# Performance work log

Measured on AMD Instinct MI355X. Metric: run time of the kernel, lower is better.

## Reference

```python
import jax, jax.numpy as jnp
import numpy as np

EPS = 1e-5
H = 128          # hidden_size
IN = 75          # input_size
T = 128          # seq len == window_size
B = 1024
OUT = 256        # lstm_output_size


def _bn(x, gamma, beta):
    # training-mode batch norm over the batch dim (biased variance, as in PyTorch BN)
    m = x.mean(axis=0)
    v = x.var(axis=0)
    return gamma * (x - m) * jax.lax.rsqrt(v + EPS) + beta


def _run_bnlstm_layer(xs, Wih, Whh, b, gih, bih, ghh, bhh, gc, bc):
    # xs: (T, B, D). Returns hidden stream (T, B, H).
    Bsz = xs.shape[1]
    h0 = jnp.zeros((Bsz, H), xs.dtype)
    c0 = jnp.zeros((Bsz, H), xs.dtype)

    def step(carry, x):
        h, c = carry
        gates = _bn(x @ Wih, gih, bih) + _bn(h @ Whh, ghh, bhh) + b  # (B, 4H)
        f, i, o, g = jnp.split(gates, 4, axis=1)                     # gate order f,i,o,g
        c1 = jax.nn.sigmoid(f) * c + jax.nn.sigmoid(i) * jnp.tanh(g)
        h1 = jax.nn.sigmoid(o) * jnp.tanh(_bn(c1, gc, bc))
        return (h1, c1), h1

    (_, _), hs = jax.lax.scan(step, (h0, c0), xs)
    return hs


def setup_inputs() -> dict:
    key = jax.random.key(0)
    ks = jax.random.split(key, 12)
    s = 0.05
    d = {
        'sequences': jax.random.normal(ks[0], (B, T, IN), jnp.float32),
        # layer 0 BNLSTM cell params (weights stored as (in, 4H) so y = x @ W)
        'Wih0': jax.random.normal(ks[1], (IN, 4 * H), jnp.float32) * s,
        'Whh0': jax.random.normal(ks[2], (H, 4 * H), jnp.float32) * s,
        'b0': jnp.zeros((4 * H,), jnp.float32),
        'gih0': jnp.full((4 * H,), 0.1, jnp.float32),
        'bih0': jnp.zeros((4 * H,), jnp.float32),
        'ghh0': jnp.full((4 * H,), 0.1, jnp.float32),
        'bhh0': jnp.zeros((4 * H,), jnp.float32),
        'gc0': jnp.full((H,), 0.1, jnp.float32),
        'bc0': jnp.zeros((H,), jnp.float32),
        # layer 1
        'Wih1': jax.random.normal(ks[3], (H, 4 * H), jnp.float32) * s,
        'Whh1': jax.random.normal(ks[4], (H, 4 * H), jnp.float32) * s,
        'b1': jnp.zeros((4 * H,), jnp.float32),
        'gih1': jnp.full((4 * H,), 0.1, jnp.float32),
        'bih1': jnp.zeros((4 * H,), jnp.float32),
        'ghh1': jnp.full((4 * H,), 0.1, jnp.float32),
        'bhh1': jnp.zeros((4 * H,), jnp.float32),
        'gc1': jnp.full((H,), 0.1, jnp.float32),
        'bc1': jnp.zeros((H,), jnp.float32),
        # fc: hidden -> lstm_output_size; decoder: lstm_output_size -> T*IN
        'fc_w': jax.random.normal(ks[5], (H, OUT), jnp.float32) * s,
        'fc_b': jnp.zeros((OUT,), jnp.float32),
        'dec_w': jax.random.normal(ks[6], (OUT, T * IN), jnp.float32) * s,
        'dec_b': jnp.zeros((T * IN,), jnp.float32),
    }
    return d


def reference(sequences, Wih0, Whh0, b0, gih0, bih0, ghh0, bhh0, gc0, bc0,
              Wih1, Whh1, b1, gih1, bih1, ghh1, bhh1, gc1, bc1,
              fc_w, fc_b, dec_w, dec_b):
    xs = jnp.transpose(sequences, (1, 0, 2))  # (T, B, IN), time-major
    hs0 = _run_bnlstm_layer(xs, Wih0, Whh0, b0, gih0, bih0, ghh0, bhh0, gc0, bc0)
    hs1 = _run_bnlstm_layer(hs0, Wih1, Whh1, b1, gih1, bih1, ghh1, bhh1, gc1, bc1)
    last = hs1[-1]                       # (B, H): last time step of top layer
    emb = last @ fc_w + fc_b             # (B, OUT)
    out = emb @ dec_w + dec_b            # (B, T*IN)
    return out.reshape(-1, T, IN)
```

## Files before the change

### kernel.cpp

```cpp
#include <hip/hip_runtime.h>
#include <stdint.h>
#include <stddef.h>

#define TT   128
#define BB   1024
#define INN  75
#define HH   128
#define KXP  96
#define OUTN 256
#define DECN 9600
#define EPSB 1e-5f

typedef short v8s __attribute__((ext_vector_type(8)));
typedef float v4f __attribute__((ext_vector_type(4)));
typedef unsigned short ush;
typedef unsigned int   u32;
typedef unsigned long long u64;

__device__ __align__(256) ush g_xpad[(size_t)TT * BB * KXP];
__device__ __align__(256) u64 g_h0s[(size_t)TT * BB * 32];
__device__ __align__(256) u64 g_h1s[(size_t)TT * BB * 32];
__device__ __align__(256) float g_c0[HH * BB];
__device__ __align__(256) float g_c1[HH * BB];
__device__ __align__(256) float g_P[(size_t)4 * 128 * 1024 * 4];
__device__ __align__(256) float g_pst[32 * 16 * 4 * 16 * 2];
__device__ __align__(256) ush g_wtih0[512 * KXP];
__device__ __align__(256) ush g_wthh0[512 * HH];
__device__ __align__(256) ush g_wtih1[512 * HH];
__device__ __align__(256) ush g_wthh1[512 * HH];
__device__ __align__(256) ush g_fcwt[OUTN * HH];
__device__ __align__(256) ush g_decwt[(size_t)DECN * OUTN];
__device__ __align__(256) ush g_emb[BB * OUTN];

__device__ __forceinline__ ush f2bf(float f) {
  u32 u = __float_as_uint(f);
  u32 r = (u + 0x7FFFu + ((u >> 16) & 1u)) >> 16;
  return (ush)r;
}
__device__ __forceinline__ float sigf(float x)  { return 1.f / (1.f + __expf(-x)); }
__device__ __forceinline__ float tanhf_(float x){ float e = __expf(2.f * x); return 1.f - 2.f / (e + 1.f); }
__device__ __forceinline__ v8s ld8(const ush* p) { return *reinterpret_cast<const v8s*>(p); }
__device__ __forceinline__ int origcol(int m) { return (m & 3) * 128 + (m >> 4) * 4 + ((m >> 2) & 3); }

__global__ void kpackx(const float* __restrict__ seq) {
  int idx = blockIdx.x * 256 + threadIdx.x;
  int kk = idx % KXP; int rest = idx / KXP;
  int b = rest % BB;  int t = rest / BB;
  float v = (kk < INN) ? seq[((size_t)b * TT + t) * INN + kk] : 0.f;
  g_xpad[idx] = f2bf(v);
}

__global__ void kpackw(const float* __restrict__ Wih0, const float* __restrict__ Whh0,
                       const float* __restrict__ Wih1, const float* __restrict__ Whh1,
                       const float* __restrict__ fcw,  const float* __restrict__ decw) {
  int idx = blockIdx.x * 256 + threadIdx.x;
  if (idx < 49152) {
    int m = idx / KXP, k = idx % KXP;
    g_wtih0[idx] = f2bf((k < INN) ? Wih0[k * 512 + origcol(m)] : 0.f);
  } else if (idx < 114688) {
    int j = idx - 49152; int m = j / HH, k = j % HH;
    g_wthh0[j] = f2bf(Whh0[k * 512 + origcol(m)]);
  } else if (idx < 180224) {
    int j = idx - 114688; int m = j / HH, k = j % HH;
    g_wtih1[j] = f2bf(Wih1[k * 512 + origcol(m)]);
  } else if (idx < 245760) {
    int j = idx - 180224; int m = j / HH, k = j % HH;
    g_wthh1[j] = f2bf(Whh1[k * 512 + origcol(m)]);
  } else if (idx < 278528) {
    int j = idx - 245760; int c = j / HH, k = j % HH;
    g_fcwt[j] = f2bf(fcw[k * OUTN + c]);
  } else {
    int j = idx - 278528; int n = j % DECN, k = j / DECN;
    g_decwt[(size_t)n * OUTN + k] = f2bf(decw[(size_t)k * DECN + n]);
  }
}

__global__ __launch_bounds__(256, 2) void kA(int s) {
  const int tid = threadIdx.x;
  const int wv = tid >> 6, l = tid & 63;
  const int lm = l & 15, lq = l >> 4;
  const int c = blockIdx.x & 31, r16 = blockIdx.x >> 5;
  const int R0 = r16 * 64 + wv * 16;
  const int row = R0 + lm;

  __shared__ float sred[4][16][8];

  const bool aL0 = (s < TT), ah0 = (s >= 1), ah1 = (s >= 2);
  const ush* const h0r = reinterpret_cast<const ush*>(g_h0s);
  const ush* const h1r = reinterpret_cast<const ush*>(g_h1s);

  v8s afx[3], af0[4], af1[4], af2[4];
#pragma unroll
  for (int ks = 0; ks < 3; ++ks)
    afx[ks] = ld8(&g_wtih0[(c * 16 + lm) * KXP + ks * 32 + lq * 8]);
#pragma unroll
  for (int ks = 0; ks < 4; ++ks) {
    af0[ks] = ld8(&g_wthh0[(c * 16 + lm) * HH + ks * 32 + lq * 8]);
    af1[ks] = ld8(&g_wtih1[(c * 16 + lm) * HH + ks * 32 + lq * 8]);
    af2[ks] = ld8(&g_wthh1[(c * 16 + lm) * HH + ks * 32 + lq * 8]);
  }

  const v4f vz = {0.f, 0.f, 0.f, 0.f};
  v4f Pi0 = vz, P0 = vz, P1 = vz, P2 = vz;

  if (aL0) {
    const ush* xp = g_xpad + ((size_t)s * BB + row) * KXP + lq * 8;
#pragma unroll
    for (int ks = 0; ks < 3; ++ks)
      Pi0 = __builtin_amdgcn_mfma_f32_16x16x32_bf16(afx[ks], ld8(xp + ks * 32), Pi0, 0, 0, 0);
  }
  if (ah0) {
    const ush* hp = h0r + ((size_t)(s - 1) * BB + row) * HH + lq * 8;
#pragma unroll
    for (int ks = 0; ks < 4; ++ks) {
      v8s b = ld8(hp + ks * 32);
      P0 = __builtin_amdgcn_mfma_f32_16x16x32_bf16(af0[ks], b, P0, 0, 0, 0);
      P1 = __builtin_amdgcn_mfma_f32_16x16x32_bf16(af1[ks], b, P1, 0, 0, 0);
    }
  }
  if (ah1) {
    const ush* hp = h1r + ((size_t)(s - 2) * BB + row) * HH + lq * 8;
#pragma unroll
    for (int ks = 0; ks < 4; ++ks)
      P2 = __builtin_amdgcn_mfma_f32_16x16x32_bf16(af2[ks], ld8(hp + ks * 32), P2, 0, 0, 0);
  }

  const int unit = c * 4 + lq;
  *reinterpret_cast<v4f*>(&g_P[((size_t)(0 * 128 + unit) * 1024 + row) * 4]) = Pi0;
  *reinterpret_cast<v4f*>(&g_P[((size_t)(1 * 128 + unit) * 1024 + row) * 4]) = P0;
  *reinterpret_cast<v4f*>(&g_P[((size_t)(2 * 128 + unit) * 1024 + row) * 4]) = P1;
  *reinterpret_cast<v4f*>(&g_P[((size_t)(3 * 128 + unit) * 1024 + row) * 4]) = P2;

  float S[4][4], Q[4][4];
#pragma unroll
  for (int r = 0; r < 4; ++r) {
    S[0][r] = Pi0[r]; Q[0][r] = Pi0[r] * Pi0[r];
    S[1][r] = P0[r];  Q[1][r] = P0[r] * P0[r];
    S[2][r] = P1[r];  Q[2][r] = P1[r] * P1[r];
    S[3][r] = P2[r];  Q[3][r] = P2[r] * P2[r];
  }
#pragma unroll
  for (int st = 0; st < 4; ++st)
#pragma unroll
    for (int r = 0; r < 4; ++r) {
      float s_ = S[st][r], q_ = Q[st][r];
#pragma unroll
      for (int off = 1; off < 16; off <<= 1) { s_ += __shfl_xor(s_, off); q_ += __shfl_xor(q_, off); }
      S[st][r] = s_; Q[st][r] = q_;
    }
  if (lm == 0)
#pragma unroll
    for (int st = 0; st < 4; ++st)
#pragma unroll
      for (int r = 0; r < 4; ++r) {
        sred[wv][lq * 4 + r][st * 2]     = S[st][r];
        sred[wv][lq * 4 + r][st * 2 + 1] = Q[st][r];
      }
  __syncthreads();
  if (tid < 16) {
#pragma unroll
    for (int st = 0; st < 4; ++st) {
      float Sa = 0.f, Qa = 0.f;
#pragma unroll
      for (int w4 = 0; w4 < 4; ++w4) { Sa += sred[w4][tid][st * 2]; Qa += sred[w4][tid][st * 2 + 1]; }
      int base = (((c * 16 + r16) * 4 + st) * 16 + tid) * 2;
      g_pst[base] = Sa; g_pst[base + 1] = Qa;
    }
  }
}

__global__ __launch_bounds__(512, 2) void kB(
    int s,
    const float* __restrict__ gih0, const float* __restrict__ bih0,
    const float* __restrict__ b0,
    const float* __restrict__ ghh0, const float* __restrict__ bhh0,
    const float* __restrict__ gc0,  const float* __restrict__ bc0,
    const float* __restrict__ gih1, const float* __restrict__ bih1,
    const float* __restrict__ ghh1, const float* __restrict__ bhh1,
    const float* __restrict__ b1,   const float* __restrict__ gc1,
    const float* __restrict__ bc1) {
  const int L = blockIdx.x >> 5, g = blockIdx.x & 31;
  if (L == 0 && s >= TT) return;
  if (L == 1 && s < 1) return;

  const int tid = threadIdx.x;
  const int wv = tid >> 6, l = tid & 63;
  const int uloc = tid & 3;
  const int rgrp = tid >> 2;
  const int unit = g * 4 + uloc;

  __shared__ float scoef[16][3];
  __shared__ float scred[8][4][2];
  __shared__ float sccoef[4][2];

  if (tid < 16) {
    const int cb = tid;
    const int stb = L * 2;
    float S0 = 0.f, Q0 = 0.f, S1 = 0.f, Q1 = 0.f;
#pragma unroll
    for (int r16 = 0; r16 < 16; ++r16) {
      int b0i = (((g * 16 + r16) * 4 + stb) * 16 + cb) * 2;
      int b1i = (((g * 16 + r16) * 4 + stb + 1) * 16 + cb) * 2;
      S0 += g_pst[b0i]; Q0 += g_pst[b0i + 1];
      S1 += g_pst[b1i]; Q1 += g_pst[b1i + 1];
    }
    const int oc = origcol(g * 16 + cb);
    float mi = S0 * (1.f / BB), vi = Q0 * (1.f / BB) - mi * mi;
    float mh = S1 * (1.f / BB), vh = Q1 * (1.f / BB) - mh * mh;
    float Ai, Ah, D;
    if (L == 0) {
      Ai = gih0[oc] * rsqrtf(vi + EPSB);
      Ah = ghh0[oc] * rsqrtf(vh + EPSB);
      D = bih0[oc] - Ai * mi + bhh0[oc] - Ah * mh + b0[oc];
    } else {
      Ai = gih1[oc] * rsqrtf(vi + EPSB);
      Ah = ghh1[oc] * rsqrtf(vh + EPSB);
      D = bih1[oc] - Ai * mi + bhh1[oc] - Ah * mh + b1[oc];
    }
    scoef[cb][0] = Ai; scoef[cb][1] = Ah; scoef[cb][2] = D;
  }
  __syncthreads();

  float AI[4], AH[4], DD[4];
#pragma unroll
  for (int r = 0; r < 4; ++r) {
    AI[r] = scoef[uloc * 4 + r][0];
    AH[r] = scoef[uloc * 4 + r][1];
    DD[r] = scoef[uloc * 4 + r][2];
  }

  const int stb = L * 2;
  const float* Pih = &g_P[(size_t)((stb * 128 + unit) * 1024) * 4];
  const float* Phh = &g_P[(size_t)(((stb + 1) * 128 + unit) * 1024) * 4];
  float* cptr = (L == 0) ? &g_c0[unit * BB] : &g_c1[unit * BB];
  const bool cold0 = (L == 0) ? (s == 0) : (s == 1);

  float cst[8], so[8];
  float cS = 0.f, cQ = 0.f;
#pragma unroll
  for (int i = 0; i < 8; ++i) {
    const int row = rgrp * 8 + i;
    v4f pih = *reinterpret_cast<const v4f*>(&Pih[row * 4]);
    v4f phh = *reinterpret_cast<const v4f*>(&Phh[row * 4]);
    float gf = AI[0] * pih[0] + AH[0] * phh[0] + DD[0];
    float gi = AI[1] * pih[1] + AH[1] * phh[1] + DD[1];
    float go = AI[2] * pih[2] + AH[2] * phh[2] + DD[2];
    float gg = AI[3] * pih[3] + AH[3] * phh[3] + DD[3];
    float cold = cold0 ? 0.f : cptr[row];
    float c1 = sigf(gf) * cold + sigf(gi) * tanhf_(gg);
    cst[i] = c1; so[i] = sigf(go);
    cptr[row] = c1;
    cS += c1; cQ += c1 * c1;
  }

#pragma unroll
  for (int off = 4; off < 64; off <<= 1) { cS += __shfl_xor(cS, off); cQ += __shfl_xor(cQ, off); }
  if (l < 4) { scred[wv][l][0] = cS; scred[wv][l][1] = cQ; }
  __syncthreads();
  if (tid < 4) {
    float S = 0.f, Q = 0.f;
#pragma unroll
    for (int w8 = 0; w8 < 8; ++w8) { S += scred[w8][tid][0]; Q += scred[w8][tid][1]; }
    float m_ = S * (1.f / BB), v_ = Q * (1.f / BB) - m_ * m_;
    int uu = g * 4 + tid;
    float gcv = (L == 0) ? gc0[uu] : gc1[uu];
    float bcv = (L == 0) ? bc0[uu] : bc1[uu];
    float ac = gcv * rsqrtf(v_ + EPSB);
    sccoef[tid][0] = ac; sccoef[tid][1] = bcv - ac * m_;
  }
  __syncthreads();
  const float ac = sccoef[uloc][0], dc = sccoef[uloc][1];

  u64* hdst = (L == 0) ? &g_h0s[(size_t)s * BB * 32] : &g_h1s[(size_t)(s - 1) * BB * 32];
#pragma unroll
  for (int i = 0; i < 8; ++i) {
    const int row = rgrp * 8 + i;
    u32 v = (u32)f2bf(so[i] * tanhf_(ac * cst[i] + dc));
    u32 a = v | (__shfl_xor(v, 1) << 16);
    u32 b = __shfl_xor(a, 2);
    if (uloc == 0) hdst[(size_t)row * 32 + g] = (u64)a | ((u64)b << 32);
  }
}

__global__ __launch_bounds__(256) void kfc(const float* __restrict__ fcb) {
  const int tid = threadIdx.x, w = tid >> 6, l = tid & 63;
  const int lm = l & 15, lq = l >> 4;
  const int col = blockIdx.x * 16 + lm;
  const ush* hsrc = reinterpret_cast<const ush*>(g_h1s) + (size_t)(TT - 1) * BB * HH;
  v8s bf[4];
#pragma unroll
  for (int ks = 0; ks < 4; ++ks) bf[ks] = ld8(&g_fcwt[col * HH + ks * 32 + lq * 8]);
  const float bias = fcb[col];
  const v4f vz = {0.f, 0.f, 0.f, 0.f};
#pragma unroll
  for (int mt = 0; mt < 16; ++mt) {
    const int rowa = w * 256 + mt * 16 + lm;
    const ush* ap = hsrc + (size_t)rowa * HH + lq * 8;
    v4f acc = vz;
#pragma unroll
    for (int ks = 0; ks < 4; ++ks)
      acc = __builtin_amdgcn_mfma_f32_16x16x32_bf16(ld8(ap + ks * 32), bf[ks], acc, 0, 0, 0);
#pragma unroll
    for (int r = 0; r < 4; ++r) {
      int row = w * 256 + mt * 16 + lq * 4 + r;
      g_emb[row * OUTN + col] = f2bf(acc[r] + bias);
    }
  }
}

__global__ __launch_bounds__(256) void kdec(const float* __restrict__ decb, float* __restrict__ out) {
  const int tid = threadIdx.x, wv = tid >> 6, l = tid & 63;
  const int lm = l & 15, lq = l >> 4;
  const int c0 = blockIdx.x * 16;
  const int R0 = wv * 256;
  v8s af[8];
#pragma unroll
  for (int ks = 0; ks < 8; ++ks) af[ks] = ld8(&g_decwt[(size_t)(c0 + lm) * OUTN + ks * 32 + lq * 8]);
  float bias[4];
#pragma unroll
  for (int r = 0; r < 4; ++r) bias[r] = decb[c0 + lq * 4 + r];
  const v4f vz = {0.f, 0.f, 0.f, 0.f};
#pragma unroll
  for (int mt = 0; mt < 16; ++mt) {
    const int row = R0 + mt * 16 + lm;
    const ush* bp = g_emb + (size_t)row * OUTN + lq * 8;
    v4f acc = vz;
#pragma unroll
    for (int ks = 0; ks < 8; ++ks)
      acc = __builtin_amdgcn_mfma_f32_16x16x32_bf16(af[ks], ld8(bp + ks * 32), acc, 0, 0, 0);
    v4f o;
#pragma unroll
    for (int r = 0; r < 4; ++r) o[r] = acc[r] + bias[r];
    *reinterpret_cast<v4f*>(&out[(size_t)row * DECN + c0 + lq * 4]) = o;
  }
}

extern "C" void kernel_launch(void* const* d_in, const int* in_sizes, int n_in,
                              void* d_out, int out_size, void* d_ws, size_t ws_size,
                              hipStream_t stream) {
  const float* seq  = (const float*)d_in[0];
  const float* Wih0 = (const float*)d_in[1];
  const float* Whh0 = (const float*)d_in[2];
  const float* b0   = (const float*)d_in[3];
  const float* gih0 = (const float*)d_in[4];
  const float* bih0 = (const float*)d_in[5];
  const float* ghh0 = (const float*)d_in[6];
  const float* bhh0 = (const float*)d_in[7];
  const float* gc0  = (const float*)d_in[8];
  const float* bc0  = (const float*)d_in[9];
  const float* Wih1 = (const float*)d_in[10];
  const float* Whh1 = (const float*)d_in[11];
  const float* b1   = (const float*)d_in[12];
  const float* gih1 = (const float*)d_in[13];
  const float* bih1 = (const float*)d_in[14];
  const float* ghh1 = (const float*)d_in[15];
  const float* bhh1 = (const float*)d_in[16];
  const float* gc1  = (const float*)d_in[17];
  const float* bc1  = (const float*)d_in[18];
  const float* fcw  = (const float*)d_in[19];
  const float* fcb  = (const float*)d_in[20];
  const float* decw = (const float*)d_in[21];
  const float* decb = (const float*)d_in[22];
  float* out = (float*)d_out;
  (void)in_sizes; (void)n_in; (void)out_size; (void)d_ws; (void)ws_size;

  kpackx<<<dim3((TT * BB * KXP) / 256), dim3(256), 0, stream>>>(seq);
  kpackw<<<dim3(10688), dim3(256), 0, stream>>>(Wih0, Whh0, Wih1, Whh1, fcw, decw);
  for (int s = 0; s <= TT; ++s) {
    kA<<<dim3(512), dim3(256), 0, stream>>>(s);
    kB<<<dim3(64), dim3(512), 0, stream>>>(s, gih0, bih0, b0, ghh0, bhh0, gc0, bc0,
                                           gih1, bih1, ghh1, bhh1, b1, gc1, bc1);
  }
  kfc<<<dim3(16), dim3(256), 0, stream>>>(fcb);
  kdec<<<dim3(600), dim3(256), 0, stream>>>(decb, out);
}
```

Measured before the change: 3.174 ms.

## Precompute layer-0 input projection and its batch norm for all timesteps up front

Adds a kprep kernel that computes x@Wih0 for every timestep in one batched MFMA pass, applies its batch norm there, and stores the normalized result as bf16 in g_G1. This takes the input GEMM and its statistics off the serial recurrent path. kA now does only three hidden-state GEMMs, and kB reads the precomputed gates. The P and cell-state buffers also get a new layout that groups units per block. The cost is a large extra buffer, extra bf16 rounding of the normalized input gates, and a new up-front kernel.

```diff
diff --git a/kernel.cpp b/kernel.cpp
--- a/kernel.cpp
+++ b/kernel.cpp
@@ -18,12 +18,12 @@
 typedef unsigned long long u64;
 
 __device__ __align__(256) ush g_xpad[(size_t)TT * BB * KXP];
+__device__ __align__(256) u64 g_G1[(size_t)TT * 32 * BB * 4];
 __device__ __align__(256) u64 g_h0s[(size_t)TT * BB * 32];
 __device__ __align__(256) u64 g_h1s[(size_t)TT * BB * 32];
-__device__ __align__(256) float g_c0[HH * BB];
-__device__ __align__(256) float g_c1[HH * BB];
-__device__ __align__(256) float g_P[(size_t)4 * 128 * 1024 * 4];
-__device__ __align__(256) float g_pst[32 * 16 * 4 * 16 * 2];
+__device__ __align__(256) float g_c[(size_t)2 * 32 * BB * 4];
+__device__ __align__(256) float g_P[(size_t)3 * 32 * BB * 16];
+__device__ __align__(256) float g_pst[32 * 16 * 3 * 16 * 2];
 __device__ __align__(256) ush g_wtih0[512 * KXP];
 __device__ __align__(256) ush g_wthh0[512 * HH];
 __device__ __align__(256) ush g_wtih1[512 * HH];
@@ -37,6 +37,7 @@
   u32 r = (u + 0x7FFFu + ((u >> 16) & 1u)) >> 16;
   return (ush)r;
 }
+__device__ __forceinline__ float bf2f(ush u) { return __uint_as_float(((u32)u) << 16); }
 __device__ __forceinline__ float sigf(float x)  { return 1.f / (1.f + __expf(-x)); }
 __device__ __forceinline__ float tanhf_(float x){ float e = __expf(2.f * x); return 1.f - 2.f / (e + 1.f); }
 __device__ __forceinline__ v8s ld8(const ush* p) { return *reinterpret_cast<const v8s*>(p); }
@@ -75,24 +76,109 @@
   }
 }
 
+__global__ __launch_bounds__(512) void kprep(const float* __restrict__ gih0,
+                                             const float* __restrict__ bih0,
+                                             const float* __restrict__ b0) {
+  const int t = blockIdx.x >> 3, ct = blockIdx.x & 7;
+  const int tid = threadIdx.x, wv = tid >> 6, l = tid & 63;
+  const int lm = l & 15, lq = l >> 4;
+  const int R0 = wv * 128;
+  __shared__ float sred[8][64][2];
+  __shared__ float scoef[64][2];
+
+  v8s af[4][3];
+#pragma unroll
+  for (int tt = 0; tt < 4; ++tt)
+#pragma unroll
+    for (int ks = 0; ks < 3; ++ks)
+      af[tt][ks] = ld8(&g_wtih0[(ct * 64 + tt * 16 + lm) * KXP + ks * 32 + lq * 8]);
+
+  const v4f vz = {0.f, 0.f, 0.f, 0.f};
+  v4f acc[8][4];
+#pragma unroll
+  for (int mt = 0; mt < 8; ++mt)
+#pragma unroll
+    for (int tt = 0; tt < 4; ++tt) acc[mt][tt] = vz;
+
+#pragma unroll
+  for (int mt = 0; mt < 8; ++mt) {
+    const ush* xr = g_xpad + ((size_t)t * BB + R0 + mt * 16 + lm) * KXP + lq * 8;
+    v8s bx0 = ld8(xr), bx1 = ld8(xr + 32), bx2 = ld8(xr + 64);
+#pragma unroll
+    for (int tt = 0; tt < 4; ++tt) {
+      acc[mt][tt] = __builtin_amdgcn_mfma_f32_16x16x32_bf16(af[tt][0], bx0, acc[mt][tt], 0, 0, 0);
+      acc[mt][tt] = __builtin_amdgcn_mfma_f32_16x16x32_bf16(af[tt][1], bx1, acc[mt][tt], 0, 0, 0);
+      acc[mt][tt] = __builtin_amdgcn_mfma_f32_16x16x32_bf16(af[tt][2], bx2, acc[mt][tt], 0, 0, 0);
+    }
+  }
+  float S[4][4], Q[4][4];
+#pragma unroll
+  for (int tt = 0; tt < 4; ++tt)
+#pragma unroll
+    for (int r = 0; r < 4; ++r) {
+      float s = 0.f, q = 0.f;
+#pragma unroll
+      for (int mt = 0; mt < 8; ++mt) { float a = acc[mt][tt][r]; s += a; q += a * a; }
+#pragma unroll
+      for (int off = 1; off < 16; off <<= 1) { s += __shfl_xor(s, off); q += __shfl_xor(q, off); }
+      S[tt][r] = s; Q[tt][r] = q;
+    }
+  if (lm == 0)
+#pragma unroll
+    for (int tt = 0; tt < 4; ++tt)
+#pragma unroll
+      for (int r = 0; r < 4; ++r) {
+        sred[wv][tt * 16 + lq * 4 + r][0] = S[tt][r];
+        sred[wv][tt * 16 + lq * 4 + r][1] = Q[tt][r];
+      }
+  __syncthreads();
+  if (tid < 64) {
+    float Sa = 0.f, Qa = 0.f;
+#pragma unroll
+    for (int w8 = 0; w8 < 8; ++w8) { Sa += sred[w8][tid][0]; Qa += sred[w8][tid][1]; }
+    int oc = origcol(ct * 64 + tid);
+    float m_ = Sa * (1.f / BB), v_ = Qa * (1.f / BB) - m_ * m_;
+    float A = gih0[oc] * rsqrtf(v_ + EPSB);
+    scoef[tid][0] = A; scoef[tid][1] = bih0[oc] - A * m_ + b0[oc];
+  }
+  __syncthreads();
+  float CA[4][4], CD[4][4];
+#pragma unroll
+  for (int tt = 0; tt < 4; ++tt)
+#pragma unroll
+    for (int r = 0; r < 4; ++r) {
+      CA[tt][r] = scoef[tt * 16 + lq * 4 + r][0];
+      CD[tt][r] = scoef[tt * 16 + lq * 4 + r][1];
+    }
+#pragma unroll
+  for (int mt = 0; mt < 8; ++mt) {
+    const int row = R0 + mt * 16 + lm;
+#pragma unroll
+    for (int tt = 0; tt < 4; ++tt) {
+      const int g = ct * 4 + tt;
+      u32 lo = (u32)f2bf(CA[tt][0] * acc[mt][tt][0] + CD[tt][0])
+             | ((u32)f2bf(CA[tt][1] * acc[mt][tt][1] + CD[tt][1]) << 16);
+      u32 hi = (u32)f2bf(CA[tt][2] * acc[mt][tt][2] + CD[tt][2])
+             | ((u32)f2bf(CA[tt][3] * acc[mt][tt][3] + CD[tt][3]) << 16);
+      g_G1[(((size_t)t * 32 + g) * BB + row) * 4 + lq] = (u64)lo | ((u64)hi << 32);
+    }
+  }
+}
+
 __global__ __launch_bounds__(256, 2) void kA(int s) {
   const int tid = threadIdx.x;
   const int wv = tid >> 6, l = tid & 63;
   const int lm = l & 15, lq = l >> 4;
   const int c = blockIdx.x & 31, r16 = blockIdx.x >> 5;
-  const int R0 = r16 * 64 + wv * 16;
-  const int row = R0 + lm;
-
-  __shared__ float sred[4][16][8];
-
-  const bool aL0 = (s < TT), ah0 = (s >= 1), ah1 = (s >= 2);
+  const int row = r16 * 64 + wv * 16 + lm;
+
+  __shared__ float sred[4][16][6];
+
+  const bool h0ok = (s >= 1), h1ok = (s >= 2);
   const ush* const h0r = reinterpret_cast<const ush*>(g_h0s);
   const ush* const h1r = reinterpret_cast<const ush*>(g_h1s);
 
-  v8s afx[3], af0[4], af1[4], af2[4];
-#pragma unroll
-  for (int ks = 0; ks < 3; ++ks)
-    afx[ks] = ld8(&g_wtih0[(c * 16 + lm) * KXP + ks * 32 + lq * 8]);
+  v8s af0[4], af1[4], af2[4];
 #pragma unroll
   for (int ks = 0; ks < 4; ++ks) {
     af0[ks] = ld8(&g_wthh0[(c * 16 + lm) * HH + ks * 32 + lq * 8]);
@@ -101,15 +187,9 @@
   }
 
   const v4f vz = {0.f, 0.f, 0.f, 0.f};
-  v4f Pi0 = vz, P0 = vz, P1 = vz, P2 = vz;
-
-  if (aL0) {
-    const ush* xp = g_xpad + ((size_t)s * BB + row) * KXP + lq * 8;
-#pragma unroll
-    for (int ks = 0; ks < 3; ++ks)
-      Pi0 = __builtin_amdgcn_mfma_f32_16x16x32_bf16(afx[ks], ld8(xp + ks * 32), Pi0, 0, 0, 0);
-  }
-  if (ah0) {
+  v4f P0 = vz, P1 = vz, P2 = vz;
+
+  if (h0ok) {
     const ush* hp = h0r + ((size_t)(s - 1) * BB + row) * HH + lq * 8;
 #pragma unroll
     for (int ks = 0; ks < 4; ++ks) {
@@ -118,29 +198,29 @@
       P1 = __builtin_amdgcn_mfma_f32_16x16x32_bf16(af1[ks], b, P1, 0, 0, 0);
     }
   }
-  if (ah1) {
+  if (h1ok) {
     const ush* hp = h1r + ((size_t)(s - 2) * BB + row) * HH + lq * 8;
 #pragma unroll
     for (int ks = 0; ks < 4; ++ks)
       P2 = __builtin_amdgcn_mfma_f32_16x16x32_bf16(af2[ks], ld8(hp + ks * 32), P2, 0, 0, 0);
   }
 
-  const int unit = c * 4 + lq;
-  *reinterpret_cast<v4f*>(&g_P[((size_t)(0 * 128 + unit) * 1024 + row) * 4]) = Pi0;
-  *reinterpret_cast<v4f*>(&g_P[((size_t)(1 * 128 + unit) * 1024 + row) * 4]) = P0;
-  *reinterpret_cast<v4f*>(&g_P[((size_t)(2 * 128 + unit) * 1024 + row) * 4]) = P1;
-  *reinterpret_cast<v4f*>(&g_P[((size_t)(3 * 128 + unit) * 1024 + row) * 4]) = P2;
-
-  float S[4][4], Q[4][4];
+  if (s < TT)
+    *reinterpret_cast<v4f*>(&g_P[(((size_t)0 * 32 + c) * BB + row) * 16 + lq * 4]) = P0;
+  if (s >= 1) {
+    *reinterpret_cast<v4f*>(&g_P[(((size_t)1 * 32 + c) * BB + row) * 16 + lq * 4]) = P1;
+    *reinterpret_cast<v4f*>(&g_P[(((size_t)2 * 32 + c) * BB + row) * 16 + lq * 4]) = P2;
+  }
+
+  float S[3][4], Q[3][4];
 #pragma unroll
   for (int r = 0; r < 4; ++r) {
-    S[0][r] = Pi0[r]; Q[0][r] = Pi0[r] * Pi0[r];
-    S[1][r] = P0[r];  Q[1][r] = P0[r] * P0[r];
-    S[2][r] = P1[r];  Q[2][r] = P1[r] * P1[r];
-    S[3][r] = P2[r];  Q[3][r] = P2[r] * P2[r];
-  }
-#pragma unroll
-  for (int st = 0; st < 4; ++st)
+    S[0][r] = P0[r]; Q[0][r] = P0[r] * P0[r];
+    S[1][r] = P1[r]; Q[1][r] = P1[r] * P1[r];
+    S[2][r] = P2[r]; Q[2][r] = P2[r] * P2[r];
+  }
+#pragma unroll
+  for (int st = 0; st < 3; ++st)
 #pragma unroll
     for (int r = 0; r < 4; ++r) {
       float s_ = S[st][r], q_ = Q[st][r];
@@ -150,7 +230,7 @@
     }
   if (lm == 0)
 #pragma unroll
-    for (int st = 0; st < 4; ++st)
+    for (int st = 0; st < 3; ++st)
 #pragma unroll
       for (int r = 0; r < 4; ++r) {
         sred[wv][lq * 4 + r][st * 2]     = S[st][r];
@@ -159,11 +239,11 @@
   __syncthreads();
   if (tid < 16) {
 #pragma unroll
-    for (int st = 0; st < 4; ++st) {
+    for (int st = 0; st < 3; ++st) {
       float Sa = 0.f, Qa = 0.f;
 #pragma unroll
       for (int w4 = 0; w4 < 4; ++w4) { Sa += sred[w4][tid][st * 2]; Qa += sred[w4][tid][st * 2 + 1]; }
-      int base = (((c * 16 + r16) * 4 + st) * 16 + tid) * 2;
+      int base = (((c * 16 + r16) * 3 + st) * 16 + tid) * 2;
       g_pst[base] = Sa; g_pst[base + 1] = Qa;
     }
   }
@@ -171,8 +251,6 @@
 
 __global__ __launch_bounds__(512, 2) void kB(
     int s,
-    const float* __restrict__ gih0, const float* __restrict__ bih0,
-    const float* __restrict__ b0,
     const float* __restrict__ ghh0, const float* __restrict__ bhh0,
     const float* __restrict__ gc0,  const float* __restrict__ bc0,
     const float* __restrict__ gih1, const float* __restrict__ bih1,
@@ -187,7 +265,6 @@
   const int wv = tid >> 6, l = tid & 63;
   const int uloc = tid & 3;
   const int rgrp = tid >> 2;
-  const int unit = g * 4 + uloc;
 
   __shared__ float scoef[16][3];
   __shared__ float scred[8][4][2];
@@ -195,61 +272,74 @@
 
   if (tid < 16) {
     const int cb = tid;
-    const int stb = L * 2;
-    float S0 = 0.f, Q0 = 0.f, S1 = 0.f, Q1 = 0.f;
-#pragma unroll
-    for (int r16 = 0; r16 < 16; ++r16) {
-      int b0i = (((g * 16 + r16) * 4 + stb) * 16 + cb) * 2;
-      int b1i = (((g * 16 + r16) * 4 + stb + 1) * 16 + cb) * 2;
-      S0 += g_pst[b0i]; Q0 += g_pst[b0i + 1];
-      S1 += g_pst[b1i]; Q1 += g_pst[b1i + 1];
-    }
     const int oc = origcol(g * 16 + cb);
-    float mi = S0 * (1.f / BB), vi = Q0 * (1.f / BB) - mi * mi;
-    float mh = S1 * (1.f / BB), vh = Q1 * (1.f / BB) - mh * mh;
-    float Ai, Ah, D;
     if (L == 0) {
-      Ai = gih0[oc] * rsqrtf(vi + EPSB);
-      Ah = ghh0[oc] * rsqrtf(vh + EPSB);
-      D = bih0[oc] - Ai * mi + bhh0[oc] - Ah * mh + b0[oc];
+      float S = 0.f, Q = 0.f;
+#pragma unroll
+      for (int r16 = 0; r16 < 16; ++r16) {
+        int bi = (((g * 16 + r16) * 3 + 0) * 16 + cb) * 2;
+        S += g_pst[bi]; Q += g_pst[bi + 1];
+      }
+      float m_ = S * (1.f / BB), v_ = Q * (1.f / BB) - m_ * m_;
+      float Ah = ghh0[oc] * rsqrtf(v_ + EPSB);
+      scoef[cb][0] = Ah; scoef[cb][1] = bhh0[oc] - Ah * m_;
     } else {
-      Ai = gih1[oc] * rsqrtf(vi + EPSB);
-      Ah = ghh1[oc] * rsqrtf(vh + EPSB);
-      D = bih1[oc] - Ai * mi + bhh1[oc] - Ah * mh + b1[oc];
-    }
-    scoef[cb][0] = Ai; scoef[cb][1] = Ah; scoef[cb][2] = D;
-  }
-  __syncthreads();
-
-  float AI[4], AH[4], DD[4];
+      float S1 = 0.f, Q1 = 0.f, S2 = 0.f, Q2 = 0.f;
+#pragma unroll
+      for (int r16 = 0; r16 < 16; ++r16) {
+        int b1i = (((g * 16 + r16) * 3 + 1) * 16 + cb) * 2;
+        int b2i = (((g * 16 + r16) * 3 + 2) * 16 + cb) * 2;
+        S1 += g_pst[b1i]; Q1 += g_pst[b1i + 1];
+        S2 += g_pst[b2i]; Q2 += g_pst[b2i + 1];
+      }
+      float m1 = S1 * (1.f / BB), v1 = Q1 * (1.f / BB) - m1 * m1;
+      float Ai = gih1[oc] * rsqrtf(v1 + EPSB);
+      float m2 = S2 * (1.f / BB), v2 = Q2 * (1.f / BB) - m2 * m2;
+      float Ah = ghh1[oc] * rsqrtf(v2 + EPSB);
+      scoef[cb][0] = Ai; scoef[cb][1] = Ah;
+      scoef[cb][2] = bih1[oc] - Ai * m1 + bhh1[oc] - Ah * m2 + b1[oc];
+    }
+  }
+  __syncthreads();
+
+  float C0[4], C1[4], C2[4];
 #pragma unroll
   for (int r = 0; r < 4; ++r) {
-    AI[r] = scoef[uloc * 4 + r][0];
-    AH[r] = scoef[uloc * 4 + r][1];
-    DD[r] = scoef[uloc * 4 + r][2];
-  }
-
-  const int stb = L * 2;
-  const float* Pih = &g_P[(size_t)((stb * 128 + unit) * 1024) * 4];
-  const float* Phh = &g_P[(size_t)(((stb + 1) * 128 + unit) * 1024) * 4];
-  float* cptr = (L == 0) ? &g_c0[unit * BB] : &g_c1[unit * BB];
+    C0[r] = scoef[uloc * 4 + r][0];
+    C1[r] = scoef[uloc * 4 + r][1];
+    C2[r] = scoef[uloc * 4 + r][2];
+  }
+
+  float* cptr = &g_c[((size_t)(L * 32 + g) * BB) * 4];
   const bool cold0 = (L == 0) ? (s == 0) : (s == 1);
+  const float* Pa = &g_P[(((size_t)(L == 0 ? 0 : 1) * 32 + g) * BB) * 16];
+  const float* Pb = &g_P[(((size_t)2 * 32 + g) * BB) * 16];
+  const u64*   G1p = &g_G1[(((size_t)s * 32 + g) * BB) * 4];
 
   float cst[8], so[8];
   float cS = 0.f, cQ = 0.f;
 #pragma unroll
   for (int i = 0; i < 8; ++i) {
     const int row = rgrp * 8 + i;
-    v4f pih = *reinterpret_cast<const v4f*>(&Pih[row * 4]);
-    v4f phh = *reinterpret_cast<const v4f*>(&Phh[row * 4]);
-    float gf = AI[0] * pih[0] + AH[0] * phh[0] + DD[0];
-    float gi = AI[1] * pih[1] + AH[1] * phh[1] + DD[1];
-    float go = AI[2] * pih[2] + AH[2] * phh[2] + DD[2];
-    float gg = AI[3] * pih[3] + AH[3] * phh[3] + DD[3];
-    float cold = cold0 ? 0.f : cptr[row];
+    float gf, gi, go, gg;
+    v4f pa = *reinterpret_cast<const v4f*>(&Pa[row * 16 + uloc * 4]);
+    if (L == 0) {
+      u64 g1 = G1p[row * 4 + uloc];
+      gf = bf2f((ush)g1)         + C0[0] * pa[0] + C1[0];
+      gi = bf2f((ush)(g1 >> 16)) + C0[1] * pa[1] + C1[1];
+      go = bf2f((ush)(g1 >> 32)) + C0[2] * pa[2] + C1[2];
+      gg = bf2f((ush)(g1 >> 48)) + C0[3] * pa[3] + C1[3];
+    } else {
+      v4f pb = *reinterpret_cast<const v4f*>(&Pb[row * 16 + uloc * 4]);
+      gf = C0[0] * pa[0] + C1[0] * pb[0] + C2[0];
+      gi = C0[1] * pa[1] + C1[1] * pb[1] + C2[1];
+      go = C0[2] * pa[2] + C1[2] * pb[2] + C2[2];
+      gg = C0[3] * pa[3] + C1[3] * pb[3] + C2[3];
+    }
+    float cold = cold0 ? 0.f : cptr[row * 4 + uloc];
     float c1 = sigf(gf) * cold + sigf(gi) * tanhf_(gg);
     cst[i] = c1; so[i] = sigf(go);
-    cptr[row] = c1;
+    cptr[row * 4 + uloc] = c1;
     cS += c1; cQ += c1 * c1;
   }
 
@@ -366,9 +456,10 @@
 
   kpackx<<<dim3((TT * BB * KXP) / 256), dim3(256), 0, stream>>>(seq);
   kpackw<<<dim3(10688), dim3(256), 0, stream>>>(Wih0, Whh0, Wih1, Whh1, fcw, decw);
+  kprep<<<dim3(TT * 8), dim3(512), 0, stream>>>(gih0, bih0, b0);
   for (int s = 0; s <= TT; ++s) {
     kA<<<dim3(512), dim3(256), 0, stream>>>(s);
-    kB<<<dim3(64), dim3(512), 0, stream>>>(s, gih0, bih0, b0, ghh0, bhh0, gc0, bc0,
+    kB<<<dim3(64), dim3(512), 0, stream>>>(s, ghh0, bhh0, gc0, bc0,
                                            gih1, bih1, ghh1, bhh1, b1, gc1, bc1);
   }
   kfc<<<dim3(16), dim3(256), 0, stream>>>(fcb);
```

Result: faster. 2.722 ms (-14.3%).
